# Kernel tuning notes

Measured on AMD Instinct MI355X. Metric: run time of the kernel, lower is better.

The kernel has to match this reference:

```python
import jax, jax.numpy as jnp
import numpy as np


def setup_inputs() -> dict:
    key = jax.random.key(0)
    ks = jax.random.split(key, 8)
    N, D, E, R = 300000, 64, 1000000, 100000
    all_emb = jax.random.normal(ks[0], (N, D), jnp.float32)
    # xavier-ish init for the edge MLP (Linear(2D->D), Linear(D->1))
    W1 = jax.random.normal(ks[1], (D, 2 * D), jnp.float32) / np.sqrt(2.0 * D).astype(np.float32)
    b1 = jnp.zeros((D,), jnp.float32)
    W2 = jax.random.normal(ks[2], (1, D), jnp.float32) / np.sqrt(1.0 * D).astype(np.float32)
    b2 = jnp.zeros((1,), jnp.float32)
    edge_index = jax.random.randint(ks[3], (2, E), 0, N, jnp.int32)
    rand_idx = jax.random.randint(ks[4], (2, R), 0, N, jnp.int32)
    eps_u = jax.random.uniform(ks[5], (E, 1), jnp.float32)
    rb_u = jax.random.uniform(ks[6], (E,), jnp.float32)
    return dict(all_emb=all_emb, W1=W1, b1=b1, W2=W2, b2=b2,
                edge_index=edge_index, rand_idx=rand_idx, eps_u=eps_u, rb_u=rb_u)


def reference(all_emb, W1, b1, W2, b2, edge_index, rand_idx, eps_u, rb_u):
    src, dst = edge_index[0], edge_index[1]
    # gather + concat: [E, 2D]
    edge_emb = jnp.concatenate([all_emb[src], all_emb[dst]], axis=1)
    h = jax.nn.relu(edge_emb @ W1.T + b1)            # [E, D]
    edge_logits = h @ W2.T + b2                      # [E, 1]
    # Gumbel-sigmoid gate, temperature 1.0; eps ~ U(bias, 1-bias)
    bias = 1e-4
    eps = (bias - (1.0 - bias)) * eps_u + (1.0 - bias)
    gate = jnp.log(eps) - jnp.log1p(-eps) + edge_logits
    edge_weight = jax.nn.sigmoid(gate)[:, 0]         # [E]
    # __build_prob_neighbourhood: RelaxedBernoulli(temp=0.9, probs=clamp(w,.01,.99)).rsample()
    att = jnp.clip(edge_weight, 0.01, 0.99)
    u = jnp.clip(rb_u, 1e-7, 1.0 - 1e-7)
    t = 0.9
    sample = jax.nn.sigmoid((jnp.log(att) - jnp.log1p(-att) + jnp.log(u) - jnp.log1p(-u)) / t)
    mask = jax.lax.stop_gradient((sample > 0.0).astype(sample.dtype))
    mat = sample * mask
    # sparse rebuild: (edge_index, mat) + graph_random (rand_idx, 0.05), then coalesce
    rand_vals = jnp.full((rand_idx.shape[1],), 0.05, mat.dtype)
    rows = jnp.concatenate([src, rand_idx[0]])
    cols = jnp.concatenate([dst, rand_idx[1]])
    vals = jnp.concatenate([mat, rand_vals])
    order = jnp.lexsort((cols, rows))                # sort by (row, col)
    rows_s, cols_s, vals_s = rows[order], cols[order], vals[order]
    change = jnp.concatenate([jnp.ones((1,), bool),
                              (rows_s[1:] != rows_s[:-1]) | (cols_s[1:] != cols_s[:-1])])
    seg = jnp.cumsum(change) - 1                     # run id per sorted entry
    sums = jax.ops.segment_sum(vals_s, seg, num_segments=vals.shape[0])
    # coalesced value placed at first occurrence of each unique (row,col); dups zeroed
    out_vals = jnp.where(change, sums[seg], 0.0)
    return rows_s, cols_s, out_vals
```

## Files before the change

### kernel.cpp

```cpp
#include <hip/hip_runtime.h>
#include <stdint.h>

typedef unsigned short u16;
typedef unsigned int   u32;
typedef __attribute__((ext_vector_type(8))) short bf16x8;
typedef __attribute__((ext_vector_type(4))) float f32x4;

__device__ __forceinline__ float bflo(u32 u){ return __uint_as_float(u << 16); }
__device__ __forceinline__ u32 f2bf(float f){
  u32 u = __float_as_uint(f);
  return (u + 0x7fffu + ((u >> 16) & 1u)) >> 16;
}
__device__ __forceinline__ float qbf(float f){ return __uint_as_float(f2bf(f) << 16); }

__global__ void k_zero(int* __restrict__ c, int N){
  int i = blockIdx.x * 256 + threadIdx.x;
  if (i < N) c[i] = 0;
}

__global__ void k_hist(const int* __restrict__ src, const int* __restrict__ rand0,
                       int* __restrict__ cnt, int E, int M){
  int i = blockIdx.x * 256 + threadIdx.x;
  if (i >= M) return;
  int row = (i < E) ? src[i] : rand0[i - E];
  atomicAdd(&cnt[row], 1);
}

__global__ void k_scan1(int* __restrict__ cnt, int* __restrict__ bsum, int N){
  __shared__ int sh[256];
  int blk = blockIdx.x, tid = threadIdx.x;
  int base = blk * 1024 + tid * 4;
  int v0 = (base + 0 < N) ? cnt[base + 0] : 0;
  int v1 = (base + 1 < N) ? cnt[base + 1] : 0;
  int v2 = (base + 2 < N) ? cnt[base + 2] : 0;
  int v3 = (base + 3 < N) ? cnt[base + 3] : 0;
  int tot = v0 + v1 + v2 + v3;
  sh[tid] = tot;
  __syncthreads();
  for (int off = 1; off < 256; off <<= 1){
    int t2 = (tid >= off) ? sh[tid - off] : 0;
    __syncthreads();
    sh[tid] += t2;
    __syncthreads();
  }
  int excl = sh[tid] - tot;
  if (base + 0 < N) cnt[base + 0] = excl;
  if (base + 1 < N) cnt[base + 1] = excl + v0;
  if (base + 2 < N) cnt[base + 2] = excl + v0 + v1;
  if (base + 3 < N) cnt[base + 3] = excl + v0 + v1 + v2;
  if (tid == 255) bsum[blk] = sh[255];
}

__global__ void k_scan2(const int* __restrict__ bsum, int* __restrict__ boff, int NB){
  __shared__ int sh[512];
  int tid = threadIdx.x;
  int v = (tid < NB) ? bsum[tid] : 0;
  sh[tid] = v;
  __syncthreads();
  for (int off = 1; off < 512; off <<= 1){
    int t2 = (tid >= off) ? sh[tid - off] : 0;
    __syncthreads();
    sh[tid] += t2;
    __syncthreads();
  }
  boff[tid] = sh[tid] - v;
}

__global__ void k_scan3(int* __restrict__ cnt, const int* __restrict__ boff, int N){
  int add = boff[blockIdx.x];
  int base = blockIdx.x * 1024 + threadIdx.x * 4;
  #pragma unroll
  for (int q = 0; q < 4; q++)
    if (base + q < N) cnt[base + q] += add;
}

__global__ void __launch_bounds__(256) k_scatter_edges(
    const u16* __restrict__ emb, const u16* __restrict__ W1,
    const u16* __restrict__ b1, const u16* __restrict__ W2,
    const u16* __restrict__ b2,
    const int* __restrict__ src, const int* __restrict__ dst,
    const u16* __restrict__ eps_u, const u16* __restrict__ rb_u,
    int* __restrict__ cursor, u32* __restrict__ packed,
    int E, int ntiles)
{
  int lane = threadIdx.x & 63;
  int c    = lane & 15;
  int quad = lane >> 4;
  int wid  = blockIdx.x * 4 + (threadIdx.x >> 6);
  int wstride = gridDim.x * 4;

  bf16x8 bfr[4][4];
  #pragma unroll
  for (int ks = 0; ks < 4; ks++)
    #pragma unroll
    for (int t = 0; t < 4; t++)
      bfr[ks][t] = *(const bf16x8*)(W1 + (size_t)(t*16 + c)*128 + ks*32 + quad*8);

  float b1v[4], w2v[4];
  #pragma unroll
  for (int t = 0; t < 4; t++){
    b1v[t] = bflo((u32)b1[t*16 + c]);
    w2v[t] = bflo((u32)W2[t*16 + c]);
  }
  float b2v = bflo((u32)b2[0]);

  for (int tile = wid; tile < ntiles; tile += wstride){
    int e_base = tile * 16;
    int em = e_base + c; if (em >= E) em = E - 1;
    int s_m = src[em], d_m = dst[em];

    f32x4 acc0 = {0.f,0.f,0.f,0.f}, acc1 = {0.f,0.f,0.f,0.f};
    f32x4 acc2 = {0.f,0.f,0.f,0.f}, acc3 = {0.f,0.f,0.f,0.f};
    #pragma unroll
    for (int ks = 0; ks < 4; ks++){
      const u16* ap = emb + (size_t)(ks < 2 ? s_m : d_m) * 64 + (ks & 1) * 32 + quad * 8;
      bf16x8 a = *(const bf16x8*)ap;
      acc0 = __builtin_amdgcn_mfma_f32_16x16x32_bf16(a, bfr[ks][0], acc0, 0, 0, 0);
      acc1 = __builtin_amdgcn_mfma_f32_16x16x32_bf16(a, bfr[ks][1], acc1, 0, 0, 0);
      acc2 = __builtin_amdgcn_mfma_f32_16x16x32_bf16(a, bfr[ks][2], acc2, 0, 0, 0);
      acc3 = __builtin_amdgcn_mfma_f32_16x16x32_bf16(a, bfr[ks][3], acc3, 0, 0, 0);
    }
    float pr[4];
    #pragma unroll
    for (int r = 0; r < 4; r++){
      float h0 = fmaxf(acc0[r] + b1v[0], 0.f);
      float h1 = fmaxf(acc1[r] + b1v[1], 0.f);
      float h2 = fmaxf(acc2[r] + b1v[2], 0.f);
      float h3 = fmaxf(acc3[r] + b1v[3], 0.f);
      pr[r] = h0*w2v[0] + h1*w2v[1] + h2*w2v[2] + h3*w2v[3];
    }
    #pragma unroll
    for (int d = 1; d < 16; d <<= 1){
      #pragma unroll
      for (int r = 0; r < 4; r++) pr[r] += __shfl_xor(pr[r], d);
    }
    int srcl = (lane & 48) | (quad * 4 + (c & 3));
    int s_e = __shfl(s_m, srcl);
    int d_e = __shfl(d_m, srcl);
    if (c < 4){
      int e = e_base + quad * 4 + c;
      if (e < E){
        float logit = ((c==0)?pr[0]:(c==1)?pr[1]:(c==2)?pr[2]:pr[3]) + b2v;
        float ue  = bflo((u32)eps_u[e]);
        float eps = fmaf(-0.9998f, ue, 0.9999f);
        float gate = (__log2f(eps) - __log2f(1.0f - eps)) * 0.69314718f + logit;
        gate = fminf(fmaxf(gate, -4.59511985f), 4.59511985f);
        float uu = fminf(fmaxf(bflo((u32)rb_u[e]), 1e-7f), 1.0f - 1e-7f);
        float lu = (__log2f(uu) - __log2f(1.0f - uu)) * 0.69314718f;
        float l  = (gate + lu) * (1.0f / 0.9f);
        float ee = __builtin_amdgcn_exp2f(-l * 1.44269504f);
        float val = 1.0f / (1.0f + ee);
        u32 h = f2bf(val);
        u32 code = (h >= 8192u) ? (h - 8192u) : 0u;
        int pos = atomicAdd(&cursor[s_e], 1);
        packed[pos] = ((u32)d_e << 13) | code;
      }
    }
  }
}

__global__ void k_scatter_rand(const int* __restrict__ rand0, const int* __restrict__ rand1,
                               int* __restrict__ cursor, u32* __restrict__ packed, int R){
  int i = blockIdx.x * 256 + threadIdx.x;
  if (i >= R) return;
  int pos = atomicAdd(&cursor[rand0[i]], 1);
  packed[pos] = ((u32)rand1[i] << 13) | 7501u;
}

__global__ void k_emit(const int* __restrict__ cursor, u32* __restrict__ packed,
                       float* __restrict__ out, int N, int M){
  int r = blockIdx.x * 256 + threadIdx.x;
  if (r >= N) return;
  int b = (r == 0) ? 0 : cursor[r - 1];
  int e = cursor[r];
  for (int i = b + 1; i < e; i++){
    u32 p = packed[i];
    int j = i - 1;
    while (j >= b && packed[j] > p){ packed[j+1] = packed[j]; j--; }
    packed[j+1] = p;
  }
  float rf = qbf((float)r);
  int i = b;
  while (i < e){
    u32 p = packed[i];
    u32 col = p >> 13;
    u32 lo  = p & 8191u;
    float sum = __uint_as_float((lo ? lo + 8192u : 0u) << 16);
    int j = i + 1;
    while (j < e && (packed[j] >> 13) == col){
      u32 l2 = packed[j] & 8191u;
      sum += __uint_as_float((l2 ? l2 + 8192u : 0u) << 16);
      j++;
    }
    float cf = qbf((float)col);
    out[i] = rf; out[M + i] = cf; out[2 * M + i] = qbf(sum);
    for (int q = i + 1; q < j; q++){
      out[q] = rf; out[M + q] = cf; out[2 * M + q] = 0.f;
    }
    i = j;
  }
}

extern "C" void kernel_launch(void* const* d_in, const int* in_sizes, int n_in,
                              void* d_out, int out_size, void* d_ws, size_t ws_size,
                              hipStream_t stream){
  (void)n_in; (void)out_size; (void)ws_size;
  const u16* all_emb = (const u16*)d_in[0];
  const u16* W1   = (const u16*)d_in[1];
  const u16* b1   = (const u16*)d_in[2];
  const u16* W2   = (const u16*)d_in[3];
  const u16* b2   = (const u16*)d_in[4];
  const int* edge_index = (const int*)d_in[5];
  const int* rand_idx   = (const int*)d_in[6];
  const u16* eps_u = (const u16*)d_in[7];
  const u16* rb_u  = (const u16*)d_in[8];

  int N = in_sizes[0] / 64;
  int E = in_sizes[5] / 2;
  int R = in_sizes[6] / 2;
  int M = E + R;
  const int* src   = edge_index;
  const int* dst   = edge_index + E;
  const int* rand0 = rand_idx;
  const int* rand1 = rand_idx + R;

  int* cnt  = (int*)d_ws;
  int* bsum = cnt + N;
  int* boff = bsum + 512;
  u32* packed = (u32*)(boff + 512);

  k_zero<<<(N + 255) / 256, 256, 0, stream>>>(cnt, N);
  k_hist<<<(M + 255) / 256, 256, 0, stream>>>(src, rand0, cnt, E, M);
  int NB = (N + 1023) / 1024;
  k_scan1<<<NB, 256, 0, stream>>>(cnt, bsum, N);
  k_scan2<<<1, 512, 0, stream>>>(bsum, boff, NB);
  k_scan3<<<NB, 256, 0, stream>>>(cnt, boff, N);
  int ntiles = (E + 15) / 16;
  k_scatter_edges<<<2048, 256, 0, stream>>>(all_emb, W1, b1, W2, b2, src, dst,
                                            eps_u, rb_u, cnt, packed, E, ntiles);
  k_scatter_rand<<<(R + 255) / 256, 256, 0, stream>>>(rand0, rand1, cnt, packed, R);
  k_emit<<<(N + 255) / 256, 256, 0, stream>>>(cnt, packed, (float*)d_out, N, M);
}
```

Before: 287.3 us.

## Fuse row histogram into edge MLP kernel and scatter codes in a separate pass

The edge MLP now runs before the prefix scan and builds the row histogram itself, covering both edges and random entries. It writes a compact 16-bit gate code per edge, and a new combined kernel scatters edges and random entries into the CSR buffer. Each wave also processes two 16-edge tiles per iteration, issuing all gathers up front to hide latency. This removes the separate histogram kernel and the random-scatter launch, at the cost of an extra codes array pass and re-reading src/dst in the scatter.

After: 311.5 us. 8.4% more time.

```diff
diff --git a/kernel.cpp b/kernel.cpp
--- a/kernel.cpp
+++ b/kernel.cpp
@@ -16,14 +16,6 @@
 __global__ void k_zero(int* __restrict__ c, int N){
   int i = blockIdx.x * 256 + threadIdx.x;
   if (i < N) c[i] = 0;
-}
-
-__global__ void k_hist(const int* __restrict__ src, const int* __restrict__ rand0,
-                       int* __restrict__ cnt, int E, int M){
-  int i = blockIdx.x * 256 + threadIdx.x;
-  if (i >= M) return;
-  int row = (i < E) ? src[i] : rand0[i - E];
-  atomicAdd(&cnt[row], 1);
 }
 
 __global__ void k_scan1(int* __restrict__ cnt, int* __restrict__ bsum, int N){
@@ -74,14 +66,15 @@
     if (base + q < N) cnt[base + q] += add;
 }
 
-__global__ void __launch_bounds__(256) k_scatter_edges(
+__global__ void __launch_bounds__(256) k_mlp_hist(
     const u16* __restrict__ emb, const u16* __restrict__ W1,
     const u16* __restrict__ b1, const u16* __restrict__ W2,
     const u16* __restrict__ b2,
     const int* __restrict__ src, const int* __restrict__ dst,
     const u16* __restrict__ eps_u, const u16* __restrict__ rb_u,
-    int* __restrict__ cursor, u32* __restrict__ packed,
-    int E, int ntiles)
+    const int* __restrict__ rand0,
+    int* __restrict__ cnt, u16* __restrict__ codes,
+    int E, int R, int ntp)
 {
   int lane = threadIdx.x & 63;
   int c    = lane & 15;
@@ -89,6 +82,12 @@
   int wid  = blockIdx.x * 4 + (threadIdx.x >> 6);
   int wstride = gridDim.x * 4;
 
+  {
+    int gtid = blockIdx.x * 256 + threadIdx.x;
+    int gsz  = gridDim.x * 256;
+    for (int i = gtid; i < R; i += gsz) atomicAdd(&cnt[rand0[i]], 1);
+  }
+
   bf16x8 bfr[4][4];
   #pragma unroll
   for (int ks = 0; ks < 4; ks++)
@@ -104,43 +103,68 @@
   }
   float b2v = bflo((u32)b2[0]);
 
-  for (int tile = wid; tile < ntiles; tile += wstride){
-    int e_base = tile * 16;
-    int em = e_base + c; if (em >= E) em = E - 1;
-    int s_m = src[em], d_m = dst[em];
-
-    f32x4 acc0 = {0.f,0.f,0.f,0.f}, acc1 = {0.f,0.f,0.f,0.f};
-    f32x4 acc2 = {0.f,0.f,0.f,0.f}, acc3 = {0.f,0.f,0.f,0.f};
+  for (int tp = wid; tp < ntp; tp += wstride){
+    int e_base = tp * 32;
+    int idx = e_base + (lane & 31);
+    if (idx >= E) idx = E - 1;
+    int nd = (lane < 32) ? src[idx] : dst[idx];
+    if (lane < 32 && (e_base + lane) < E) atomicAdd(&cnt[nd], 1);
+
+    int s0 = __shfl(nd, c),      d0 = __shfl(nd, 32 + c);
+    int s1 = __shfl(nd, 16 + c), d1 = __shfl(nd, 48 + c);
+
+    bf16x8 a0[4], a1[4];
     #pragma unroll
     for (int ks = 0; ks < 4; ks++){
-      const u16* ap = emb + (size_t)(ks < 2 ? s_m : d_m) * 64 + (ks & 1) * 32 + quad * 8;
-      bf16x8 a = *(const bf16x8*)ap;
-      acc0 = __builtin_amdgcn_mfma_f32_16x16x32_bf16(a, bfr[ks][0], acc0, 0, 0, 0);
-      acc1 = __builtin_amdgcn_mfma_f32_16x16x32_bf16(a, bfr[ks][1], acc1, 0, 0, 0);
-      acc2 = __builtin_amdgcn_mfma_f32_16x16x32_bf16(a, bfr[ks][2], acc2, 0, 0, 0);
-      acc3 = __builtin_amdgcn_mfma_f32_16x16x32_bf16(a, bfr[ks][3], acc3, 0, 0, 0);
-    }
-    float pr[4];
+      a0[ks] = *(const bf16x8*)(emb + (size_t)(ks < 2 ? s0 : d0) * 64 + (ks & 1) * 32 + quad * 8);
+      a1[ks] = *(const bf16x8*)(emb + (size_t)(ks < 2 ? s1 : d1) * 64 + (ks & 1) * 32 + quad * 8);
+    }
+
+    f32x4 acc0[4], acc1[4];
+    #pragma unroll
+    for (int t = 0; t < 4; t++){
+      acc0[t] = (f32x4){0.f,0.f,0.f,0.f};
+      acc1[t] = (f32x4){0.f,0.f,0.f,0.f};
+    }
+    #pragma unroll
+    for (int ks = 0; ks < 4; ks++){
+      #pragma unroll
+      for (int t = 0; t < 4; t++){
+        acc0[t] = __builtin_amdgcn_mfma_f32_16x16x32_bf16(a0[ks], bfr[ks][t], acc0[t], 0, 0, 0);
+        acc1[t] = __builtin_amdgcn_mfma_f32_16x16x32_bf16(a1[ks], bfr[ks][t], acc1[t], 0, 0, 0);
+      }
+    }
+
+    float pr0[4], pr1[4];
     #pragma unroll
     for (int r = 0; r < 4; r++){
-      float h0 = fmaxf(acc0[r] + b1v[0], 0.f);
-      float h1 = fmaxf(acc1[r] + b1v[1], 0.f);
-      float h2 = fmaxf(acc2[r] + b1v[2], 0.f);
-      float h3 = fmaxf(acc3[r] + b1v[3], 0.f);
-      pr[r] = h0*w2v[0] + h1*w2v[1] + h2*w2v[2] + h3*w2v[3];
+      float h0 = fmaxf(acc0[0][r] + b1v[0], 0.f);
+      float h1 = fmaxf(acc0[1][r] + b1v[1], 0.f);
+      float h2 = fmaxf(acc0[2][r] + b1v[2], 0.f);
+      float h3 = fmaxf(acc0[3][r] + b1v[3], 0.f);
+      pr0[r] = h0*w2v[0] + h1*w2v[1] + h2*w2v[2] + h3*w2v[3];
+      float g0 = fmaxf(acc1[0][r] + b1v[0], 0.f);
+      float g1 = fmaxf(acc1[1][r] + b1v[1], 0.f);
+      float g2 = fmaxf(acc1[2][r] + b1v[2], 0.f);
+      float g3 = fmaxf(acc1[3][r] + b1v[3], 0.f);
+      pr1[r] = g0*w2v[0] + g1*w2v[1] + g2*w2v[2] + g3*w2v[3];
     }
     #pragma unroll
     for (int d = 1; d < 16; d <<= 1){
       #pragma unroll
-      for (int r = 0; r < 4; r++) pr[r] += __shfl_xor(pr[r], d);
-    }
-    int srcl = (lane & 48) | (quad * 4 + (c & 3));
-    int s_e = __shfl(s_m, srcl);
-    int d_e = __shfl(d_m, srcl);
-    if (c < 4){
-      int e = e_base + quad * 4 + c;
+      for (int r = 0; r < 4; r++){
+        pr0[r] += __shfl_xor(pr0[r], d);
+        pr1[r] += __shfl_xor(pr1[r], d);
+      }
+    }
+
+    if (c < 8){
+      int tile = c >> 2, r = c & 3;
+      int e = e_base + tile * 16 + quad * 4 + r;
       if (e < E){
-        float logit = ((c==0)?pr[0]:(c==1)?pr[1]:(c==2)?pr[2]:pr[3]) + b2v;
+        float pv0 = (r==0)?pr0[0]:(r==1)?pr0[1]:(r==2)?pr0[2]:pr0[3];
+        float pv1 = (r==0)?pr1[0]:(r==1)?pr1[1]:(r==2)?pr1[2]:pr1[3];
+        float logit = (tile ? pv1 : pv0) + b2v;
         float ue  = bflo((u32)eps_u[e]);
         float eps = fmaf(-0.9998f, ue, 0.9999f);
         float gate = (__log2f(eps) - __log2f(1.0f - eps)) * 0.69314718f + logit;
@@ -152,19 +176,27 @@
         float val = 1.0f / (1.0f + ee);
         u32 h = f2bf(val);
         u32 code = (h >= 8192u) ? (h - 8192u) : 0u;
-        int pos = atomicAdd(&cursor[s_e], 1);
-        packed[pos] = ((u32)d_e << 13) | code;
+        codes[e] = (u16)code;
       }
     }
   }
 }
 
-__global__ void k_scatter_rand(const int* __restrict__ rand0, const int* __restrict__ rand1,
-                               int* __restrict__ cursor, u32* __restrict__ packed, int R){
+__global__ void k_scatter_all(const int* __restrict__ src, const int* __restrict__ dst,
+                              const u16* __restrict__ codes,
+                              const int* __restrict__ rand0, const int* __restrict__ rand1,
+                              int* __restrict__ cursor, u32* __restrict__ packed,
+                              int E, int M){
   int i = blockIdx.x * 256 + threadIdx.x;
-  if (i >= R) return;
-  int pos = atomicAdd(&cursor[rand0[i]], 1);
-  packed[pos] = ((u32)rand1[i] << 13) | 7501u;
+  if (i >= M) return;
+  int row, col; u32 code;
+  if (i < E){
+    row = src[i]; col = dst[i]; code = (u32)codes[i];
+  } else {
+    row = rand0[i - E]; col = rand1[i - E]; code = 7501u;
+  }
+  int pos = atomicAdd(&cursor[row], 1);
+  packed[pos] = ((u32)col << 13) | code;
 }
 
 __global__ void k_emit(const int* __restrict__ cursor, u32* __restrict__ packed,
@@ -228,16 +260,17 @@
   int* bsum = cnt + N;
   int* boff = bsum + 512;
   u32* packed = (u32*)(boff + 512);
+  u16* codes  = (u16*)(packed + M);
 
   k_zero<<<(N + 255) / 256, 256, 0, stream>>>(cnt, N);
-  k_hist<<<(M + 255) / 256, 256, 0, stream>>>(src, rand0, cnt, E, M);
+  int ntp = (E + 31) / 32;
+  k_mlp_hist<<<2048, 256, 0, stream>>>(all_emb, W1, b1, W2, b2, src, dst,
+                                       eps_u, rb_u, rand0, cnt, codes, E, R, ntp);
   int NB = (N + 1023) / 1024;
   k_scan1<<<NB, 256, 0, stream>>>(cnt, bsum, N);
   k_scan2<<<1, 512, 0, stream>>>(bsum, boff, NB);
   k_scan3<<<NB, 256, 0, stream>>>(cnt, boff, N);
-  int ntiles = (E + 15) / 16;
-  k_scatter_edges<<<2048, 256, 0, stream>>>(all_emb, W1, b1, W2, b2, src, dst,
-                                            eps_u, rb_u, cnt, packed, E, ntiles);
-  k_scatter_rand<<<(R + 255) / 256, 256, 0, stream>>>(rand0, rand1, cnt, packed, R);
+  k_scatter_all<<<(M + 255) / 256, 256, 0, stream>>>(src, dst, codes, rand0, rand1,
+                                                     cnt, packed, E, M);
   k_emit<<<(N + 255) / 256, 256, 0, stream>>>(cnt, packed, (float*)d_out, N, M);
 }
```
